# Performance work log

Hardware: AMD Instinct MI355X
Metric: run time of the kernel (lower is better)

The kernel has to match this reference:

```python
import jax, jax.numpy as jnp
import numpy as np

HIDDEN = 4096
N_HEADS = 32
N_KV = 8
HEAD_DIM = 128
ROPE_BASE = 10000.0


def setup_inputs() -> dict:
    key = jax.random.key(0)
    k0, k1, k2, k3, k4 = jax.random.split(key, 5)
    B, S = 1, 2048
    scale = 0.02
    return {
        "hidden_states": jax.random.normal(k0, (B, S, HIDDEN), dtype=jnp.float32),
        "Wq": jax.random.normal(k1, (N_HEADS * HEAD_DIM, HIDDEN), dtype=jnp.float32) * scale,
        "Wk": jax.random.normal(k2, (N_KV * HEAD_DIM, HIDDEN), dtype=jnp.float32) * scale,
        "Wv": jax.random.normal(k3, (N_KV * HEAD_DIM, HIDDEN), dtype=jnp.float32) * scale,
        "Wo": jax.random.normal(k4, (HIDDEN, N_HEADS * HEAD_DIM), dtype=jnp.float32) * scale,
    }


def _rotate_half(x):
    x1, x2 = jnp.split(x, 2, axis=-1)
    return jnp.concatenate([-x2, x1], axis=-1)


def _rope_cos_sin(seq_len, dtype):
    inv_freq = 1.0 / (ROPE_BASE ** (jnp.arange(0, HEAD_DIM, 2, dtype=jnp.float32) / HEAD_DIM))
    t = jnp.arange(seq_len, dtype=jnp.float32)
    freqs = jnp.outer(t, inv_freq)                 # [S, hd/2]
    emb = jnp.concatenate([freqs, freqs], axis=-1) # [S, hd]
    return jnp.cos(emb).astype(dtype), jnp.sin(emb).astype(dtype)


def reference(hidden_states, Wq, Wk, Wv, Wo):
    B, S, _ = hidden_states.shape
    scale = HEAD_DIM ** -0.5
    groups = N_HEADS // N_KV

    q = (hidden_states @ Wq.T).reshape(B, S, N_HEADS, HEAD_DIM).transpose(0, 2, 1, 3)
    k = (hidden_states @ Wk.T).reshape(B, S, N_KV, HEAD_DIM).transpose(0, 2, 1, 3)
    v = (hidden_states @ Wv.T).reshape(B, S, N_KV, HEAD_DIM).transpose(0, 2, 1, 3)

    cos, sin = _rope_cos_sin(S, q.dtype)           # [S, hd] each, broadcast over (B, H)
    q = q * cos + _rotate_half(q) * sin
    k = k * cos + _rotate_half(k) * sin

    # repeat_kv: [B, nkv, S, hd] -> [B, nkv*groups, S, hd]
    k = jnp.broadcast_to(k[:, :, None], (B, N_KV, groups, S, HEAD_DIM)).reshape(B, N_HEADS, S, HEAD_DIM)
    v = jnp.broadcast_to(v[:, :, None], (B, N_KV, groups, S, HEAD_DIM)).reshape(B, N_HEADS, S, HEAD_DIM)

    scores = jnp.einsum('bhqd,bhkd->bhqk', q, k) * scale
    causal = jnp.tril(jnp.ones((S, S), dtype=bool))
    scores = jnp.where(causal, scores, -jnp.inf)
    probs = jax.nn.softmax(scores.astype(jnp.float32), axis=-1).astype(q.dtype)

    attn = jnp.einsum('bhqk,bhkd->bhqd', probs, v)            # [B, H, S, hd]
    attn = attn.transpose(0, 2, 1, 3).reshape(B, S, N_HEADS * HEAD_DIM)
    return attn @ Wo.T
```

## Files before the change

### kernel.cpp

```cpp
#include <hip/hip_runtime.h>
#include <hip/hip_bf16.h>
#include <math.h>

#define S_LEN 2048
#define HIDDEN 4096
#define N_HEADS 32
#define N_KV 8
#define HEAD_DIM 128

typedef __attribute__((ext_vector_type(8))) short short8;
typedef __attribute__((ext_vector_type(4))) float f32x4;

typedef __attribute__((address_space(3))) unsigned int as3_u32;
typedef const __attribute__((address_space(1))) unsigned int as1_u32;

__device__ __forceinline__ void gload16(const void* g, void* lds) {
  __builtin_amdgcn_global_load_lds((as1_u32*)g, (as3_u32*)lds, 16, 0, 0);
}

__device__ __forceinline__ unsigned short f2bf(float f) {
  unsigned int u = __float_as_uint(f);
  return (unsigned short)((u + 0x7fff + ((u >> 16) & 1)) >> 16);
}
__device__ __forceinline__ float bf2f(unsigned short u) {
  return __uint_as_float(((unsigned int)u) << 16);
}

__global__ void conv_bf16(const float* __restrict__ in, unsigned short* __restrict__ out, int n) {
  int i = (blockIdx.x * blockDim.x + threadIdx.x) * 4;
  if (i >= n) return;
  float4 v = *(const float4*)&in[i];
  ushort4 o;
  o.x = f2bf(v.x); o.y = f2bf(v.y); o.z = f2bf(v.z); o.w = f2bf(v.w);
  *(ushort4*)&out[i] = o;
}

__device__ __forceinline__ void storeC(float* C, float v) { *C = v; }
__device__ __forceinline__ void storeC(unsigned short* C, float v) { *C = f2bf(v); }

template <typename OutT>
__device__ __forceinline__ void gemm_core_128(
    const unsigned short* __restrict__ A, const unsigned short* __restrict__ B,
    OutT* __restrict__ C, int K, int ldc) {
  __shared__ unsigned short As[128 * 32];
  __shared__ unsigned short Bs[128 * 32];

  const int tid = threadIdx.x;
  const int w = tid >> 6;
  const int lane = tid & 63;
  const int wr = (w >> 1) * 64;
  const int wc = (w & 1) * 64;
  const int lrow = lane & 15;
  const int lk8 = lane >> 4;

  f32x4 acc[4][4];
#pragma unroll
  for (int i = 0; i < 4; i++)
#pragma unroll
    for (int j = 0; j < 4; j++) acc[i][j] = (f32x4){0.f, 0.f, 0.f, 0.f};

  const int sr = (lane >> 2);
  const int sc = (lane & 3) * 8;

  for (int k0 = 0; k0 < K; k0 += 32) {
    __syncthreads();
#pragma unroll
    for (int s = 0; s < 2; s++) {
      int r = w * 32 + s * 16 + sr;
      gload16(&A[(size_t)r * K + k0 + sc], &As[(w * 32 + s * 16) * 32]);
      gload16(&B[(size_t)r * K + k0 + sc], &Bs[(w * 32 + s * 16) * 32]);
    }
    __syncthreads();

    short8 a[4], b[4];
#pragma unroll
    for (int i = 0; i < 4; i++)
      a[i] = *(const short8*)&As[(wr + i * 16 + lrow) * 32 + lk8 * 8];
#pragma unroll
    for (int j = 0; j < 4; j++)
      b[j] = *(const short8*)&Bs[(wc + j * 16 + lrow) * 32 + lk8 * 8];
#pragma unroll
    for (int i = 0; i < 4; i++)
#pragma unroll
      for (int j = 0; j < 4; j++)
        acc[i][j] = __builtin_amdgcn_mfma_f32_16x16x32_bf16(a[i], b[j], acc[i][j], 0, 0, 0);
  }

#pragma unroll
  for (int i = 0; i < 4; i++)
#pragma unroll
    for (int j = 0; j < 4; j++) {
      int col = wc + j * 16 + lrow;
#pragma unroll
      for (int r = 0; r < 4; r++) {
        int row = wr + i * 16 + lk8 * 4 + r;
        storeC(&C[(size_t)row * ldc + col], acc[i][j][r]);
      }
    }
}

__global__ __launch_bounds__(256) void gemm_qkv(
    const unsigned short* __restrict__ Xb,
    const unsigned short* __restrict__ Wqb, const unsigned short* __restrict__ Wkb,
    const unsigned short* __restrict__ Wvb,
    unsigned short* __restrict__ Qb, unsigned short* __restrict__ Kb,
    unsigned short* __restrict__ Vb) {
  const int colBase = blockIdx.x * 128;
  const int rowBase = blockIdx.y * 128;
  const unsigned short* B;
  unsigned short* C;
  int ldc, ccol;
  if (colBase < 4096)      { B = Wqb + (size_t)colBase * HIDDEN;          C = Qb; ldc = 4096; ccol = colBase; }
  else if (colBase < 5120) { B = Wkb + (size_t)(colBase - 4096) * HIDDEN; C = Kb; ldc = 1024; ccol = colBase - 4096; }
  else                     { B = Wvb + (size_t)(colBase - 5120) * HIDDEN; C = Vb; ldc = 1024; ccol = colBase - 5120; }
  gemm_core_128(Xb + (size_t)rowBase * HIDDEN, B,
                C + (size_t)rowBase * ldc + ccol, HIDDEN, ldc);
}

__global__ __launch_bounds__(256) void gemm_out(
    const unsigned short* __restrict__ Ob, const unsigned short* __restrict__ Wob,
    float* __restrict__ C) {
  const int colBase = blockIdx.x * 128;
  const int rowBase = blockIdx.y * 128;
  gemm_core_128(Ob + (size_t)rowBase * HIDDEN, Wob + (size_t)colBase * HIDDEN,
                C + (size_t)rowBase * HIDDEN + colBase, HIDDEN, HIDDEN);
}

#define QSCALE 0.12753102123752056f

__global__ void rope_kernel(const unsigned short* __restrict__ Q,
                            const unsigned short* __restrict__ K,
                            unsigned short* __restrict__ Qp,
                            unsigned short* __restrict__ Kp) {
  int idx = blockIdx.x * blockDim.x + threadIdx.x;
  int d = idx & 63;
  int sh = idx >> 6;
  int h = sh % (N_HEADS + N_KV);
  int s = sh / (N_HEADS + N_KV);
  if (s >= S_LEN) return;

  float freq = expf(-(float)d * (9.210340371976184f / 64.0f));
  float ang = (float)s * freq;
  float sn, cs;
  sincosf(ang, &sn, &cs);

  const unsigned short* src;
  unsigned short* dst;
  float sc_out;
  if (h < N_HEADS) {
    src = Q + ((size_t)s * N_HEADS + h) * HEAD_DIM;
    dst = Qp + (((size_t)h * 128 + (s >> 4)) * 16 + (s & 15)) * HEAD_DIM;
    sc_out = QSCALE;
  } else {
    int kvh = h - N_HEADS;
    src = K + ((size_t)s * N_KV + kvh) * HEAD_DIM;
    dst = Kp + (((size_t)kvh * 32 + (s >> 6)) * 64 + (s & 63)) * HEAD_DIM;
    sc_out = 1.0f;
  }

  float x1 = bf2f(src[d]);
  float x2 = bf2f(src[d + 64]);
  dst[d] = f2bf((x1 * cs - x2 * sn) * sc_out);
  dst[d + 64] = f2bf((x2 * cs + x1 * sn) * sc_out);
}

__global__ __launch_bounds__(256) void transp_v(
    const unsigned short* __restrict__ Vb, unsigned short* __restrict__ Vp) {
  __shared__ unsigned short t[64][72];
  const int s0 = blockIdx.x * 64;
  const int c0 = blockIdx.y * 64;
  const int kt = s0 >> 6;
  const int tid = threadIdx.x;
#pragma unroll
  for (int i = 0; i < 2; i++) {
    int c = tid + i * 256;
    int r = c >> 3, ch = c & 7;
    *(short8*)&t[r][ch * 8] = *(const short8*)&Vb[(size_t)(s0 + r) * 1024 + c0 + ch * 8];
  }
  __syncthreads();
#pragma unroll
  for (int i = 0; i < 4; i++) {
    int c = tid + i * 256;
    int orow = c >> 4, oc4 = (c & 15) * 4;
    int g = c0 + orow;
    int kvh = g >> 7, d = g & 127;
    ushort4 o;
    o.x = t[oc4 + 0][orow]; o.y = t[oc4 + 1][orow];
    o.z = t[oc4 + 2][orow]; o.w = t[oc4 + 3][orow];
    *(ushort4*)&Vp[(((size_t)kvh * 32 + kt) * 128 + d) * 64 + oc4] = o;
  }
}

#define AK 64
#define PSTR 72

__global__ __launch_bounds__(256, 3) void attn_mfma(
    const unsigned short* __restrict__ Qp, const unsigned short* __restrict__ Kp,
    const unsigned short* __restrict__ Vp, unsigned short* __restrict__ Ob) {
  const int b = blockIdx.x;
  const int h = b & 31;
  const int qi = (b < 256) ? (b >> 5) : (15 - ((b - 256) >> 5));
  const int kvh = h >> 2;

  const int tid = threadIdx.x;
  const int w = tid >> 6;
  const int lane = tid & 63;
  const int lrow = lane & 15;
  const int lk8 = lane >> 4;

  __shared__ unsigned short Ks[64 * 128];
  __shared__ unsigned short Vts[128 * 64];
  __shared__ unsigned short Ps[4 * 32 * PSTR];
  unsigned short* Pw = &Ps[w * 32 * PSTR];

  short8 qf[2][4];
  const int t0 = qi * 8 + w * 2;
#pragma unroll
  for (int i = 0; i < 2; i++)
#pragma unroll
    for (int ks = 0; ks < 4; ks++)
      qf[i][ks] = *(const short8*)&Qp[(((size_t)h * 128 + t0 + i) * 16 + lrow) * 128 +
                                      ks * 32 + lk8 * 8];

  f32x4 acc[8][2];
  float m_i[2], l_i[2];
#pragma unroll
  for (int n = 0; n < 8; n++)
#pragma unroll
    for (int i = 0; i < 2; i++) acc[n][i] = (f32x4){0.f, 0.f, 0.f, 0.f};
  m_i[0] = m_i[1] = -1e30f;
  l_i[0] = l_i[1] = 0.f;

  const int nkt = 2 * qi + 2;

  for (int kt = 0; kt < nkt; kt++) {
    const int kb = kt * AK;
    const unsigned short* Kt  = Kp + ((size_t)kvh * 32 + kt) * 8192;
    const unsigned short* Vtt = Vp + ((size_t)kvh * 32 + kt) * 8192;

    __syncthreads();
#pragma unroll
    for (int j = 0; j < 4; j++) {
      int seg = w * 4 + j;
      int kr = seg * 4 + lk8;
      int kc = lrow ^ (kr & 15);
      gload16(Kt + ((size_t)kr * 16 + kc) * 8, &Ks[seg * 512]);
      int vr = seg * 8 + (lane >> 3);
      int vc = (lane & 7) ^ (vr & 7);
      gload16(Vtt + ((size_t)vr * 8 + vc) * 8, &Vts[seg * 512]);
    }
    __syncthreads();

    f32x4 s[2][4];
#pragma unroll
    for (int i = 0; i < 2; i++)
#pragma unroll
      for (int n = 0; n < 4; n++) s[i][n] = (f32x4){0.f, 0.f, 0.f, 0.f};

#pragma unroll
    for (int ks = 0; ks < 4; ks++) {
      short8 kf[4];
#pragma unroll
      for (int n = 0; n < 4; n++)
        kf[n] = *(const short8*)&Ks[(n * 16 + lrow) * 128 + (((ks * 4 + lk8) ^ lrow)) * 8];
#pragma unroll
      for (int i = 0; i < 2; i++)
#pragma unroll
        for (int n = 0; n < 4; n++)
          s[i][n] = __builtin_amdgcn_mfma_f32_16x16x32_bf16(kf[n], qf[i][ks], s[i][n], 0, 0, 0);
    }

    const int wqb = qi * 128 + w * 32;
    if (kb + AK - 1 > wqb) {
#pragma unroll
      for (int i = 0; i < 2; i++) {
        int query = wqb + i * 16 + lrow;
#pragma unroll
        for (int n = 0; n < 4; n++) {
          int keyb = kb + n * 16 + lk8 * 4;
#pragma unroll
          for (int r = 0; r < 4; r++)
            if (keyb + r > query) s[i][n][r] = -1e30f;
        }
      }
    }

#pragma unroll
    for (int i = 0; i < 2; i++) {
      float mx = -1e30f;
#pragma unroll
      for (int n = 0; n < 4; n++)
#pragma unroll
        for (int r = 0; r < 4; r++) mx = fmaxf(mx, s[i][n][r]);
      mx = fmaxf(mx, __shfl_xor(mx, 16, 64));
      mx = fmaxf(mx, __shfl_xor(mx, 32, 64));
      float mn = fmaxf(m_i[i], mx);
      float al = exp2f(m_i[i] - mn);
      m_i[i] = mn;
      float ls = 0.f;
#pragma unroll
      for (int n = 0; n < 4; n++)
#pragma unroll
        for (int r = 0; r < 4; r++) {
          float e = exp2f(s[i][n][r] - mn);
          s[i][n][r] = e;
          ls += e;
        }
      ls += __shfl_xor(ls, 16, 64);
      ls += __shfl_xor(ls, 32, 64);
      l_i[i] = l_i[i] * al + ls;
#pragma unroll
      for (int n = 0; n < 8; n++)
#pragma unroll
        for (int r = 0; r < 4; r++) acc[n][i][r] *= al;
    }

#pragma unroll
    for (int i = 0; i < 2; i++)
#pragma unroll
      for (int n = 0; n < 4; n++) {
        ushort4 pk;
        pk.x = f2bf(s[i][n][0]); pk.y = f2bf(s[i][n][1]);
        pk.z = f2bf(s[i][n][2]); pk.w = f2bf(s[i][n][3]);
        *(ushort4*)&Pw[(i * 16 + lrow) * PSTR + n * 16 + lk8 * 4] = pk;
      }

#pragma unroll
    for (int ks2 = 0; ks2 < 2; ks2++) {
      short8 pf[2];
#pragma unroll
      for (int i = 0; i < 2; i++)
        pf[i] = *(const short8*)&Pw[(i * 16 + lrow) * PSTR + ks2 * 32 + lk8 * 8];
#pragma unroll
      for (int n = 0; n < 8; n++) {
        short8 vf = *(const short8*)&Vts[(n * 16 + lrow) * 64 +
                                         (((ks2 * 4 + lk8) ^ (lrow & 7))) * 8];
#pragma unroll
        for (int i = 0; i < 2; i++)
          acc[n][i] = __builtin_amdgcn_mfma_f32_16x16x32_bf16(vf, pf[i], acc[n][i], 0, 0, 0);
      }
    }
  }

#pragma unroll
  for (int i = 0; i < 2; i++) {
    float inv = 1.0f / l_i[i];
    int row = qi * 128 + w * 32 + i * 16 + lrow;
#pragma unroll
    for (int n = 0; n < 8; n++) {
      ushort4 o;
      o.x = f2bf(acc[n][i][0] * inv); o.y = f2bf(acc[n][i][1] * inv);
      o.z = f2bf(acc[n][i][2] * inv); o.w = f2bf(acc[n][i][3] * inv);
      *(ushort4*)&Ob[(size_t)row * 4096 + h * 128 + n * 16 + lk8 * 4] = o;
    }
  }
}

extern "C" void kernel_launch(void* const* d_in, const int* in_sizes, int n_in,
                              void* d_out, int out_size, void* d_ws, size_t ws_size,
                              hipStream_t stream) {
  const float* X  = (const float*)d_in[0];
  const float* Wq = (const float*)d_in[1];
  const float* Wk = (const float*)d_in[2];
  const float* Wv = (const float*)d_in[3];
  const float* Wo = (const float*)d_in[4];
  float* out = (float*)d_out;

  char* p = (char*)d_ws;
  unsigned short* Qb  = (unsigned short*)p; p += (size_t)S_LEN * 4096 * 2;
  unsigned short* Kb  = (unsigned short*)p; p += (size_t)S_LEN * 1024 * 2;
  unsigned short* Vb  = (unsigned short*)p; p += (size_t)S_LEN * 1024 * 2;
  unsigned short* Qp  = (unsigned short*)p; p += (size_t)S_LEN * 4096 * 2;
  unsigned short* Kp  = (unsigned short*)p; p += (size_t)S_LEN * 1024 * 2;
  unsigned short* Vp  = (unsigned short*)p; p += (size_t)S_LEN * 1024 * 2;
  unsigned short* Xb  = (unsigned short*)p; p += (size_t)S_LEN * 4096 * 2;
  unsigned short* Wqb = (unsigned short*)p; p += (size_t)4096 * 4096 * 2;
  unsigned short* Wkb = (unsigned short*)p; p += (size_t)1024 * 4096 * 2;
  unsigned short* Wvb = (unsigned short*)p; p += (size_t)1024 * 4096 * 2;
  unsigned short* Ob  = Xb;
  unsigned short* Wob = Wqb;

  conv_bf16<<<(S_LEN * 4096 / 4 + 255) / 256, 256, 0, stream>>>(X, Xb, S_LEN * 4096);
  conv_bf16<<<(4096 * 4096 / 4 + 255) / 256, 256, 0, stream>>>(Wq, Wqb, 4096 * 4096);
  conv_bf16<<<(1024 * 4096 / 4 + 255) / 256, 256, 0, stream>>>(Wk, Wkb, 1024 * 4096);
  conv_bf16<<<(1024 * 4096 / 4 + 255) / 256, 256, 0, stream>>>(Wv, Wvb, 1024 * 4096);

  gemm_qkv<<<dim3(6144 / 128, S_LEN / 128), 256, 0, stream>>>(Xb, Wqb, Wkb, Wvb, Qb, Kb, Vb);

  int rope_threads = S_LEN * (N_HEADS + N_KV) * 64;
  rope_kernel<<<rope_threads / 256, 256, 0, stream>>>(Qb, Kb, Qp, Kp);

  transp_v<<<dim3(S_LEN / 64, 1024 / 64), 256, 0, stream>>>(Vb, Vp);

  conv_bf16<<<(4096 * 4096 / 4 + 255) / 256, 256, 0, stream>>>(Wo, Wob, 4096 * 4096);

  attn_mfma<<<512, 256, 0, stream>>>(Qp, Kp, Vp, Ob);

  gemm_out<<<dim3(4096 / 128, S_LEN / 128), 256, 0, stream>>>(Ob, Wob, out);
}
```

Before: 578.2 us.

## Halve attention query tile to 64 rows and double grid size

Each attention block now handles 64 queries (16 per wave) instead of 128, so the grid doubles to 1024 blocks. Causal work is balanced by ordering tiles ascending for the first half of the grid and descending for the second. The P buffer drops its padding in favour of an XOR swizzle, and the launch bound rises to 4 blocks per CU. The aim is better occupancy and finer causal load balancing, at the cost of loading each K/V tile twice as often per query.

```diff
diff --git a/kernel.cpp b/kernel.cpp
--- a/kernel.cpp
+++ b/kernel.cpp
@@ -192,14 +192,14 @@
 }
 
 #define AK 64
-#define PSTR 72
-
-__global__ __launch_bounds__(256, 3) void attn_mfma(
+
+__global__ __launch_bounds__(256, 4) void attn_mfma(
     const unsigned short* __restrict__ Qp, const unsigned short* __restrict__ Kp,
     const unsigned short* __restrict__ Vp, unsigned short* __restrict__ Ob) {
   const int b = blockIdx.x;
   const int h = b & 31;
-  const int qi = (b < 256) ? (b >> 5) : (15 - ((b - 256) >> 5));
+  const int j = b >> 5;
+  const int qt = (b < 512) ? j : (47 - j);
   const int kvh = h >> 2;
 
   const int tid = threadIdx.x;
@@ -210,28 +210,22 @@
 
   __shared__ unsigned short Ks[64 * 128];
   __shared__ unsigned short Vts[128 * 64];
-  __shared__ unsigned short Ps[4 * 32 * PSTR];
-  unsigned short* Pw = &Ps[w * 32 * PSTR];
-
-  short8 qf[2][4];
-  const int t0 = qi * 8 + w * 2;
-#pragma unroll
-  for (int i = 0; i < 2; i++)
-#pragma unroll
-    for (int ks = 0; ks < 4; ks++)
-      qf[i][ks] = *(const short8*)&Qp[(((size_t)h * 128 + t0 + i) * 16 + lrow) * 128 +
-                                      ks * 32 + lk8 * 8];
-
-  f32x4 acc[8][2];
-  float m_i[2], l_i[2];
-#pragma unroll
-  for (int n = 0; n < 8; n++)
-#pragma unroll
-    for (int i = 0; i < 2; i++) acc[n][i] = (f32x4){0.f, 0.f, 0.f, 0.f};
-  m_i[0] = m_i[1] = -1e30f;
-  l_i[0] = l_i[1] = 0.f;
-
-  const int nkt = 2 * qi + 2;
+  __shared__ unsigned short Ps[4 * 16 * 64];
+  unsigned short* Pw = &Ps[w * 16 * 64];
+
+  short8 qf[4];
+  const int t0 = qt * 4 + w;
+#pragma unroll
+  for (int ks = 0; ks < 4; ks++)
+    qf[ks] = *(const short8*)&Qp[(((size_t)h * 128 + t0) * 16 + lrow) * 128 +
+                                 ks * 32 + lk8 * 8];
+
+  f32x4 acc[8];
+  float m_i = -1e30f, l_i = 0.f;
+#pragma unroll
+  for (int n = 0; n < 8; n++) acc[n] = (f32x4){0.f, 0.f, 0.f, 0.f};
+
+  const int nkt = qt + 1;
 
   for (int kt = 0; kt < nkt; kt++) {
     const int kb = kt * AK;
@@ -240,8 +234,8 @@
 
     __syncthreads();
 #pragma unroll
-    for (int j = 0; j < 4; j++) {
-      int seg = w * 4 + j;
+    for (int jj = 0; jj < 4; jj++) {
+      int seg = w * 4 + jj;
       int kr = seg * 4 + lk8;
       int kc = lrow ^ (kr & 15);
       gload16(Kt + ((size_t)kr * 16 + kc) * 8, &Ks[seg * 512]);
@@ -251,11 +245,9 @@
     }
     __syncthreads();
 
-    f32x4 s[2][4];
-#pragma unroll
-    for (int i = 0; i < 2; i++)
-#pragma unroll
-      for (int n = 0; n < 4; n++) s[i][n] = (f32x4){0.f, 0.f, 0.f, 0.f};
+    f32x4 s[4];
+#pragma unroll
+    for (int n = 0; n < 4; n++) s[n] = (f32x4){0.f, 0.f, 0.f, 0.f};
 
 #pragma unroll
     for (int ks = 0; ks < 4; ks++) {
@@ -264,93 +256,82 @@
       for (int n = 0; n < 4; n++)
         kf[n] = *(const short8*)&Ks[(n * 16 + lrow) * 128 + (((ks * 4 + lk8) ^ lrow)) * 8];
 #pragma unroll
-      for (int i = 0; i < 2; i++)
-#pragma unroll
-        for (int n = 0; n < 4; n++)
-          s[i][n] = __builtin_amdgcn_mfma_f32_16x16x32_bf16(kf[n], qf[i][ks], s[i][n], 0, 0, 0);
-    }
-
-    const int wqb = qi * 128 + w * 32;
+      for (int n = 0; n < 4; n++)
+        s[n] = __builtin_amdgcn_mfma_f32_16x16x32_bf16(kf[n], qf[ks], s[n], 0, 0, 0);
+    }
+
+    const int wqb = qt * 64 + w * 16;
     if (kb + AK - 1 > wqb) {
-#pragma unroll
-      for (int i = 0; i < 2; i++) {
-        int query = wqb + i * 16 + lrow;
-#pragma unroll
-        for (int n = 0; n < 4; n++) {
-          int keyb = kb + n * 16 + lk8 * 4;
-#pragma unroll
-          for (int r = 0; r < 4; r++)
-            if (keyb + r > query) s[i][n][r] = -1e30f;
-        }
+      int query = wqb + lrow;
+#pragma unroll
+      for (int n = 0; n < 4; n++) {
+        int keyb = kb + n * 16 + lk8 * 4;
+#pragma unroll
+        for (int r = 0; r < 4; r++)
+          if (keyb + r > query) s[n][r] = -1e30f;
       }
     }
 
-#pragma unroll
-    for (int i = 0; i < 2; i++) {
+    {
       float mx = -1e30f;
 #pragma unroll
       for (int n = 0; n < 4; n++)
 #pragma unroll
-        for (int r = 0; r < 4; r++) mx = fmaxf(mx, s[i][n][r]);
+        for (int r = 0; r < 4; r++) mx = fmaxf(mx, s[n][r]);
       mx = fmaxf(mx, __shfl_xor(mx, 16, 64));
       mx = fmaxf(mx, __shfl_xor(mx, 32, 64));
-      float mn = fmaxf(m_i[i], mx);
-      float al = exp2f(m_i[i] - mn);
-      m_i[i] = mn;
+      float mn = fmaxf(m_i, mx);
+      float al = exp2f(m_i - mn);
+      m_i = mn;
       float ls = 0.f;
 #pragma unroll
       for (int n = 0; n < 4; n++)
 #pragma unroll
         for (int r = 0; r < 4; r++) {
-          float e = exp2f(s[i][n][r] - mn);
-          s[i][n][r] = e;
+          float e = exp2f(s[n][r] - mn);
+          s[n][r] = e;
           ls += e;
         }
       ls += __shfl_xor(ls, 16, 64);
       ls += __shfl_xor(ls, 32, 64);
-      l_i[i] = l_i[i] * al + ls;
+      l_i = l_i * al + ls;
 #pragma unroll
       for (int n = 0; n < 8; n++)
 #pragma unroll
-        for (int r = 0; r < 4; r++) acc[n][i][r] *= al;
-    }
-
-#pragma unroll
-    for (int i = 0; i < 2; i++)
-#pragma unroll
-      for (int n = 0; n < 4; n++) {
-        ushort4 pk;
-        pk.x = f2bf(s[i][n][0]); pk.y = f2bf(s[i][n][1]);
-        pk.z = f2bf(s[i][n][2]); pk.w = f2bf(s[i][n][3]);
-        *(ushort4*)&Pw[(i * 16 + lrow) * PSTR + n * 16 + lk8 * 4] = pk;
-      }
+        for (int r = 0; r < 4; r++) acc[n][r] *= al;
+    }
+
+#pragma unroll
+    for (int n = 0; n < 4; n++) {
+      ushort4 pk;
+      pk.x = f2bf(s[n][0]); pk.y = f2bf(s[n][1]);
+      pk.z = f2bf(s[n][2]); pk.w = f2bf(s[n][3]);
+      int c8 = n * 4 + lk8;
+      int c16s = (c8 >> 1) ^ (lrow & 7);
+      *(ushort4*)&Pw[lrow * 64 + c16s * 8 + (c8 & 1) * 4] = pk;
+    }
 
 #pragma unroll
     for (int ks2 = 0; ks2 < 2; ks2++) {
-      short8 pf[2];
-#pragma unroll
-      for (int i = 0; i < 2; i++)
-        pf[i] = *(const short8*)&Pw[(i * 16 + lrow) * PSTR + ks2 * 32 + lk8 * 8];
+      int c16s = (ks2 * 4 + lk8) ^ (lrow & 7);
+      short8 pf = *(const short8*)&Pw[lrow * 64 + c16s * 8];
 #pragma unroll
       for (int n = 0; n < 8; n++) {
         short8 vf = *(const short8*)&Vts[(n * 16 + lrow) * 64 +
                                          (((ks2 * 4 + lk8) ^ (lrow & 7))) * 8];
-#pragma unroll
-        for (int i = 0; i < 2; i++)
-          acc[n][i] = __builtin_amdgcn_mfma_f32_16x16x32_bf16(vf, pf[i], acc[n][i], 0, 0, 0);
+        acc[n] = __builtin_amdgcn_mfma_f32_16x16x32_bf16(vf, pf, acc[n], 0, 0, 0);
       }
     }
   }
 
-#pragma unroll
-  for (int i = 0; i < 2; i++) {
-    float inv = 1.0f / l_i[i];
-    int row = qi * 128 + w * 32 + i * 16 + lrow;
+  {
+    float inv = 1.0f / l_i;
+    int row = qt * 64 + w * 16 + lrow;
 #pragma unroll
     for (int n = 0; n < 8; n++) {
       ushort4 o;
-      o.x = f2bf(acc[n][i][0] * inv); o.y = f2bf(acc[n][i][1] * inv);
-      o.z = f2bf(acc[n][i][2] * inv); o.w = f2bf(acc[n][i][3] * inv);
+      o.x = f2bf(acc[n][0] * inv); o.y = f2bf(acc[n][1] * inv);
+      o.z = f2bf(acc[n][2] * inv); o.w = f2bf(acc[n][3] * inv);
       *(ushort4*)&Ob[(size_t)row * 4096 + h * 128 + n * 16 + lk8 * 4] = o;
     }
   }
@@ -394,7 +375,7 @@
 
   conv_bf16<<<(4096 * 4096 / 4 + 255) / 256, 256, 0, stream>>>(Wo, Wob, 4096 * 4096);
 
-  attn_mfma<<<512, 256, 0, stream>>>(Qp, Kp, Vp, Ob);
+  attn_mfma<<<1024, 256, 0, stream>>>(Qp, Kp, Vp, Ob);
 
   gemm_out<<<dim3(4096 / 128, S_LEN / 128), 256, 0, stream>>>(Ob, Wob, out);
 }
```

After: 507.5 us. 1.14x faster.
